# Kernel tuning notes

Hardware: AMD Instinct MI355X
Metric: run time of the kernel (lower is better)

## Reference

```python
import jax, jax.numpy as jnp
import numpy as np

N_HEAD = 16
N_EMBD = 2048
HEAD_DIM = N_EMBD // N_HEAD  # 128
ROPE_THETA = 10000.0


def _make_rope(T, hd, theta):
    inv = 1.0 / (theta ** (np.arange(0, hd, 2, dtype=np.float32) / hd))  # (hd/2,)
    t = np.arange(T, dtype=np.float32)
    freqs = np.outer(t, inv)  # (T, hd/2)
    return jnp.asarray(np.cos(freqs)), jnp.asarray(np.sin(freqs))


def setup_inputs() -> dict:
    key = jax.random.key(0)
    k1, k2, k3 = jax.random.split(key, 3)
    B, T, C = 2, 2048, N_EMBD
    x = jax.random.normal(k1, (B, T, C), dtype=jnp.float32)
    cos, sin = _make_rope(T, HEAD_DIM, ROPE_THETA)
    w_qkv = jax.random.normal(k2, (3 * C, C), dtype=jnp.float32) * (1.0 / np.sqrt(C))
    w_proj = jax.random.normal(k3, (C, C), dtype=jnp.float32) * (1.0 / np.sqrt(C))
    return {"x": x, "cos": cos, "sin": sin, "w_qkv": w_qkv, "w_proj": w_proj}


def _apply_rope(x, cos, sin):
    # x: (B, H, T, hd); cos/sin: (T, hd/2). Interleaved (even/odd) RoPE.
    B, H, T, hd = x.shape
    xp = x.reshape(B, H, T, hd // 2, 2)
    x1, x2 = xp[..., 0], xp[..., 1]
    c = cos[:T][None, None, :, :]
    s = sin[:T][None, None, :, :]
    even = x1 * c - x2 * s
    odd = x1 * s + x2 * c
    return jnp.stack([even, odd], axis=-1).reshape(B, H, T, hd)


def reference(x, cos, sin, w_qkv, w_proj):
    B, T, C = x.shape
    H, hd = N_HEAD, HEAD_DIM
    qkv = jnp.einsum('btc,dc->btd', x, w_qkv)  # (B,T,3C)
    q, k, v = jnp.split(qkv, 3, axis=-1)
    # (B,T,C) -> (B,H,T,hd)
    q = q.reshape(B, T, H, hd).transpose(0, 2, 1, 3)
    k = k.reshape(B, T, H, hd).transpose(0, 2, 1, 3)
    v = v.reshape(B, T, H, hd).transpose(0, 2, 1, 3)
    q = _apply_rope(q, cos, sin)
    k = _apply_rope(k, cos, sin)
    scale = 1.0 / jnp.sqrt(jnp.asarray(hd, dtype=x.dtype))
    scores = jnp.einsum('bhqd,bhkd->bhqk', q, k) * scale  # (B,H,T,T)
    causal = jnp.tril(jnp.ones((T, T), dtype=bool))
    scores = jnp.where(causal[None, None], scores, jnp.asarray(-jnp.inf, dtype=scores.dtype))
    attn = jax.nn.softmax(scores, axis=-1)
    out = jnp.einsum('bhqk,bhkd->bhqd', attn, v)  # (B,H,T,hd)
    out = out.transpose(0, 2, 1, 3).reshape(B, T, C)
    return jnp.einsum('btc,dc->btd', out, w_proj)
```

## Files before the change

### kernel.cpp

```cpp
#include <hip/hip_runtime.h>
#include <hip/hip_bf16.h>
#include <stdint.h>

typedef __attribute__((ext_vector_type(8))) short bf16x8;
typedef __attribute__((ext_vector_type(4))) float f32x4;

#define B_ 2
#define T_ 2048
#define C_ 2048
#define H_ 16
#define HD_ 128

__device__ inline ushort f2bf(float f) {
  union { float f; uint32_t u; } v; v.f = f;
  uint32_t u = v.u;
  uint32_t r = (u + 0x7fffu + ((u >> 16) & 1u)) >> 16;
  return (ushort)r;
}
__device__ inline float bf2f(ushort h) {
  union { uint32_t u; float f; } v; v.u = ((uint32_t)h) << 16;
  return v.f;
}

typedef const __attribute__((address_space(1))) void* gas1_t;
typedef __attribute__((address_space(3))) void* las3_t;
__device__ inline void gld_lds16(const void* g, void* l) {
  __builtin_amdgcn_global_load_lds((gas1_t)g, (las3_t)l, 16, 0, 0);
}

__global__ __launch_bounds__(256) void k_f2bf(const float* __restrict__ in,
                                              ushort* __restrict__ out, int n4) {
  int i = blockIdx.x * 256 + threadIdx.x;
  if (i < n4) {
    f32x4 v = *(const f32x4*)(in + (size_t)i * 4);
    ushort4 o;
    o.x = f2bf(v[0]); o.y = f2bf(v[1]); o.z = f2bf(v[2]); o.w = f2bf(v[3]);
    *(ushort4*)(out + (size_t)i * 4) = o;
  }
}

template <int OUT_BF16>
__global__ __launch_bounds__(256)
void gemm_bt(const ushort* __restrict__ A, const ushort* __restrict__ Bm,
             void* __restrict__ Cout, int M, int N, int K) {
  __shared__ ushort lA[2][128 * 32];
  __shared__ ushort lB[2][128 * 32];
  const int tid = threadIdx.x;
  const int wid = tid >> 6, lane = tid & 63;
  const int bx = blockIdx.x, by = blockIdx.y;
  const size_t rowA0 = (size_t)by * 128, colB0 = (size_t)bx * 128;
  const int sr = lane >> 2, sc = (lane & 3) * 8;

  const ushort* Abase = A + rowA0 * K + sc;
  const ushort* Bbase = Bm + colB0 * K + sc;

  auto stage = [&](int buf, int kt) {
    const ushort* Ak = Abase + (size_t)kt * 32;
    const ushort* Bk = Bbase + (size_t)kt * 32;
    for (int i = 0; i < 2; i++) {
      int chunk = wid * 2 + i;
      int row = chunk * 16 + sr;
      gld_lds16(Ak + (size_t)row * K, &lA[buf][chunk * 512]);
      gld_lds16(Bk + (size_t)row * K, &lB[buf][chunk * 512]);
    }
  };

  f32x4 acc[4][4];
  const f32x4 zf = {0.f, 0.f, 0.f, 0.f};
  for (int i = 0; i < 4; i++)
    for (int j = 0; j < 4; j++) acc[i][j] = zf;

  const int wr = (wid >> 1) * 64, wc = (wid & 1) * 64;
  const int lr = lane & 15, lk = (lane >> 4) * 8;

  stage(0, 0);
  __syncthreads();
  const int NT = K / 32;
  int buf = 0;
  for (int kt = 0; kt < NT; kt++) {
    if (kt + 1 < NT) stage(buf ^ 1, kt + 1);
    bf16x8 af[4], bfr[4];
    for (int i = 0; i < 4; i++)
      af[i] = *(const bf16x8*)&lA[buf][(wr + i * 16 + lr) * 32 + lk];
    for (int j = 0; j < 4; j++)
      bfr[j] = *(const bf16x8*)&lB[buf][(wc + j * 16 + lr) * 32 + lk];
    for (int i = 0; i < 4; i++)
      for (int j = 0; j < 4; j++)
        acc[i][j] = __builtin_amdgcn_mfma_f32_16x16x32_bf16(af[i], bfr[j],
                                                            acc[i][j], 0, 0, 0);
    __syncthreads();
    buf ^= 1;
  }
  const int lq = (lane >> 4) * 4;
  for (int i = 0; i < 4; i++)
    for (int j = 0; j < 4; j++)
      for (int r = 0; r < 4; r++) {
        size_t row = rowA0 + wr + i * 16 + lq + r;
        size_t col = colB0 + wc + j * 16 + lr;
        float v = acc[i][j][r];
        if (OUT_BF16)
          ((ushort*)Cout)[row * (size_t)N + col] = f2bf(v);
        else
          ((float*)Cout)[row * (size_t)N + col] = v;
      }
}

__global__ __launch_bounds__(256)
void rope_split(const ushort* __restrict__ qkv, const float* __restrict__ cosb,
                const float* __restrict__ sinb, ushort* __restrict__ Qr,
                ushort* __restrict__ Kr, ushort* __restrict__ Vr) {
  const int bt = blockIdx.x;
  const int b = bt >> 11, t = bt & 2047;
  const ushort* base = qkv + (size_t)bt * (3 * C_);
  const int tid = threadIdx.x;
  const float rs = 0.08838834764831845f;
  for (int i = 0; i < 4; i++) {
    int idx = tid + i * 256;
    int h = idx >> 6, p = idx & 63;
    float c = cosb[t * 64 + p], s = sinb[t * 64 + p];
    size_t src = (size_t)h * HD_ + 2 * p;
    size_t dst = (((size_t)(b * H_ + h)) * T_ + t) * HD_ + 2 * p;
    float x1 = bf2f(base[src]), x2 = bf2f(base[src + 1]);
    Qr[dst] = f2bf((x1 * c - x2 * s) * rs);
    Qr[dst + 1] = f2bf((x1 * s + x2 * c) * rs);
    x1 = bf2f(base[C_ + src]); x2 = bf2f(base[C_ + src + 1]);
    Kr[dst] = f2bf(x1 * c - x2 * s);
    Kr[dst + 1] = f2bf(x1 * s + x2 * c);
    Vr[dst] = base[2 * C_ + src];
    Vr[dst + 1] = base[2 * C_ + src + 1];
  }
}

__global__ __launch_bounds__(256)
void attn_fwd(const ushort* __restrict__ Qr, const ushort* __restrict__ Kr,
              const ushort* __restrict__ Vr, ushort* __restrict__ Out) {
  __shared__ ushort lK[32][136];
  __shared__ ushort lV[128][40];
  __shared__ ushort lP[4][16][40];
  const int tid = threadIdx.x, wid = tid >> 6, lane = tid & 63;
  const int bh = blockIdx.y;
  const int b = bh >> 4, h = bh & 15;
  const int qt = (blockIdx.x + blockIdx.y) & 31;
  const int qbase = qt * 64 + wid * 16;
  const int lr = lane & 15, lk8 = (lane >> 4) * 8;

  const ushort* Qp = Qr + ((size_t)bh * T_ + qbase) * HD_;
  const ushort* Kp = Kr + (size_t)bh * T_ * HD_;
  const ushort* Vp = Vr + (size_t)bh * T_ * HD_;

  bf16x8 qf[4];
  for (int dc = 0; dc < 4; dc++)
    qf[dc] = *(const bf16x8*)(Qp + (size_t)lr * HD_ + dc * 32 + lk8);

  f32x4 o[8];
  const f32x4 zf = {0.f, 0.f, 0.f, 0.f};
  for (int dt = 0; dt < 8; dt++) o[dt] = zf;
  float m[4], l[4];
  for (int r = 0; r < 4; r++) { m[r] = -1e30f; l[r] = 0.f; }

  int rK[2], cK[2], rV[2], cV[2];
  for (int i = 0; i < 2; i++) {
    int chunk = tid + i * 256;
    rK[i] = chunk >> 4; cK[i] = (chunk & 15) * 8;
    rV[i] = chunk & 31; cV[i] = (chunk >> 5) * 8;
  }

  bf16x8 kreg[2], vreg[2];
  auto load_tile = [&](int kt) {
    for (int i = 0; i < 2; i++) {
      kreg[i] = *(const bf16x8*)(Kp + ((size_t)(kt * 32 + rK[i])) * HD_ + cK[i]);
      vreg[i] = *(const bf16x8*)(Vp + ((size_t)(kt * 32 + rV[i])) * HD_ + cV[i]);
    }
  };

  const int nkt = 2 * qt + 2;
  load_tile(0);
  for (int kt = 0; kt < nkt; kt++) {
    __syncthreads();
    for (int i = 0; i < 2; i++) {
      *(bf16x8*)&lK[rK[i]][cK[i]] = kreg[i];
      for (int j = 0; j < 8; j++) lV[cV[i] + j][rV[i]] = (ushort)vreg[i][j];
    }
    if (kt + 1 < nkt) load_tile(kt + 1);
    __syncthreads();
    if (kt * 32 <= qbase + 15) {
      f32x4 s[2];
      for (int kn = 0; kn < 2; kn++) {
        f32x4 a = zf;
        for (int dc = 0; dc < 4; dc++) {
          bf16x8 kf = *(const bf16x8*)&lK[kn * 16 + lr][dc * 32 + lk8];
          a = __builtin_amdgcn_mfma_f32_16x16x32_bf16(qf[dc], kf, a, 0, 0, 0);
        }
        s[kn] = a;
      }
      const int qrow = qbase + (lane >> 4) * 4;
      for (int kn = 0; kn < 2; kn++) {
        int kg = kt * 32 + kn * 16 + lr;
        for (int r = 0; r < 4; r++)
          if (kg > qrow + r) s[kn][r] = -1e30f;
      }
      float al[4];
      for (int r = 0; r < 4; r++) {
        float pm = fmaxf(s[0][r], s[1][r]);
        for (int off = 1; off < 16; off <<= 1)
          pm = fmaxf(pm, __shfl_xor(pm, off, 64));
        float mn = fmaxf(m[r], pm);
        float a = __expf(m[r] - mn);
        float p0 = __expf(s[0][r] - mn);
        float p1 = __expf(s[1][r] - mn);
        s[0][r] = p0; s[1][r] = p1;
        float rsum = p0 + p1;
        for (int off = 1; off < 16; off <<= 1)
          rsum += __shfl_xor(rsum, off, 64);
        l[r] = l[r] * a + rsum;
        m[r] = mn;
        al[r] = a;
      }
      for (int dt = 0; dt < 8; dt++)
        for (int r = 0; r < 4; r++) o[dt][r] *= al[r];
      for (int kn = 0; kn < 2; kn++)
        for (int r = 0; r < 4; r++)
          lP[wid][(lane >> 4) * 4 + r][kn * 16 + lr] = f2bf(s[kn][r]);
      bf16x8 pf = *(const bf16x8*)&lP[wid][lr][lk8];
      for (int dt = 0; dt < 8; dt++) {
        bf16x8 vf = *(const bf16x8*)&lV[dt * 16 + lr][lk8];
        o[dt] = __builtin_amdgcn_mfma_f32_16x16x32_bf16(pf, vf, o[dt], 0, 0, 0);
      }
    }
  }
  for (int r = 0; r < 4; r++) {
    float inv = 1.0f / l[r];
    int qg = qbase + (lane >> 4) * 4 + r;
    size_t obase = ((size_t)b * T_ + qg) * C_ + (size_t)h * HD_;
    for (int dt = 0; dt < 8; dt++)
      Out[obase + dt * 16 + lr] = f2bf(o[dt][r] * inv);
  }
}

extern "C" void kernel_launch(void* const* d_in, const int* in_sizes, int n_in,
                              void* d_out, int out_size, void* d_ws,
                              size_t ws_size, hipStream_t stream) {
  (void)in_sizes; (void)n_in; (void)out_size; (void)ws_size;
  const float* x = (const float*)d_in[0];
  const float* cosb = (const float*)d_in[1];
  const float* sinb = (const float*)d_in[2];
  const float* w_qkv = (const float*)d_in[3];
  const float* w_proj = (const float*)d_in[4];

  char* ws = (char*)d_ws;
  ushort* wqkvb = (ushort*)(ws);
  ushort* wprojb = (ushort*)(ws + 25165824);
  ushort* xb = (ushort*)(ws + 25165824 + 8388608);
  ushort* qkv = (ushort*)(ws + 25165824 + 8388608 + 16777216);
  ushort* kr = (ushort*)(ws + 25165824 + 8388608 + 16777216 + 50331648);
  ushort* vr = (ushort*)(ws + 25165824 + 8388608 + 16777216 + 50331648 + 16777216);
  ushort* qr = xb;
  ushort* attn_out = qkv;

  k_f2bf<<<8192, 256, 0, stream>>>(x, xb, 2097152);
  k_f2bf<<<12288, 256, 0, stream>>>(w_qkv, wqkvb, 3145728);
  k_f2bf<<<4096, 256, 0, stream>>>(w_proj, wprojb, 1048576);

  gemm_bt<1><<<dim3(48, 32), 256, 0, stream>>>(xb, wqkvb, (void*)qkv,
                                               4096, 6144, 2048);
  rope_split<<<4096, 256, 0, stream>>>(qkv, cosb, sinb, qr, kr, vr);
  attn_fwd<<<dim3(32, 32), 256, 0, stream>>>(qr, kr, vr, attn_out);
  gemm_bt<0><<<dim3(16, 32), 256, 0, stream>>>(attn_out, wprojb, d_out,
                                               4096, 2048, 2048);
}
```

Before: 499.1 us.

## Pair causal q-tiles per block, transpose MFMA operands, add lazy softmax rescale

The attention kernel now runs 16 blocks per head, and each block handles q-tile pr and q-tile 31-pr in turn, so every block gets the same causal work. The QK and PV MFMAs swap operand order, which puts one query row in each lane. That turns the row max and sum reductions into two cross-group shuffles instead of four, and allows vectorized output and P stores. An online-softmax rescale is skipped when the new max exceeds the old one by no more than 5 in every lane, which avoids the per-tile accumulator scaling. The trade-offs are half as many blocks, which may lower occupancy and latency hiding, and some numerical risk from the deferred max.

```diff
diff --git a/kernel.cpp b/kernel.cpp
--- a/kernel.cpp
+++ b/kernel.cpp
@@ -140,23 +140,12 @@
   const int tid = threadIdx.x, wid = tid >> 6, lane = tid & 63;
   const int bh = blockIdx.y;
   const int b = bh >> 4, h = bh & 15;
-  const int qt = (blockIdx.x + blockIdx.y) & 31;
-  const int qbase = qt * 64 + wid * 16;
-  const int lr = lane & 15, lk8 = (lane >> 4) * 8;
-
-  const ushort* Qp = Qr + ((size_t)bh * T_ + qbase) * HD_;
+  const int pr = blockIdx.x;
+  const int lr = lane & 15, g = lane >> 4, lk8 = g * 8;
+  const f32x4 zf = {0.f, 0.f, 0.f, 0.f};
+
   const ushort* Kp = Kr + (size_t)bh * T_ * HD_;
   const ushort* Vp = Vr + (size_t)bh * T_ * HD_;
-
-  bf16x8 qf[4];
-  for (int dc = 0; dc < 4; dc++)
-    qf[dc] = *(const bf16x8*)(Qp + (size_t)lr * HD_ + dc * 32 + lk8);
-
-  f32x4 o[8];
-  const f32x4 zf = {0.f, 0.f, 0.f, 0.f};
-  for (int dt = 0; dt < 8; dt++) o[dt] = zf;
-  float m[4], l[4];
-  for (int r = 0; r < 4; r++) { m[r] = -1e30f; l[r] = 0.f; }
 
   int rK[2], cK[2], rV[2], cV[2];
   for (int i = 0; i < 2; i++) {
@@ -165,75 +154,103 @@
     rV[i] = chunk & 31; cV[i] = (chunk >> 5) * 8;
   }
 
-  bf16x8 kreg[2], vreg[2];
-  auto load_tile = [&](int kt) {
-    for (int i = 0; i < 2; i++) {
-      kreg[i] = *(const bf16x8*)(Kp + ((size_t)(kt * 32 + rK[i])) * HD_ + cK[i]);
-      vreg[i] = *(const bf16x8*)(Vp + ((size_t)(kt * 32 + rV[i])) * HD_ + cV[i]);
+  for (int seg = 0; seg < 2; ++seg) {
+    const int qt = seg ? (31 - pr) : pr;
+    const int qbase = qt * 64 + wid * 16;
+    const ushort* Qp = Qr + ((size_t)bh * T_ + qbase) * HD_;
+
+    bf16x8 qf[4];
+    for (int dc = 0; dc < 4; dc++)
+      qf[dc] = *(const bf16x8*)(Qp + (size_t)lr * HD_ + dc * 32 + lk8);
+
+    f32x4 o[8];
+    for (int dt = 0; dt < 8; dt++) o[dt] = zf;
+    float m = -1e30f, l = 0.f;
+
+    bf16x8 kreg[2], vreg[2];
+    auto load_tile = [&](int kt) {
+      for (int i = 0; i < 2; i++) {
+        kreg[i] = *(const bf16x8*)(Kp + ((size_t)(kt * 32 + rK[i])) * HD_ + cK[i]);
+        vreg[i] = *(const bf16x8*)(Vp + ((size_t)(kt * 32 + rV[i])) * HD_ + cV[i]);
+      }
+    };
+
+    const int nkt = 2 * qt + 2;
+    load_tile(0);
+    for (int kt = 0; kt < nkt; kt++) {
+      __syncthreads();
+      for (int i = 0; i < 2; i++) {
+        *(bf16x8*)&lK[rK[i]][cK[i]] = kreg[i];
+        for (int j = 0; j < 8; j++) lV[cV[i] + j][rV[i]] = (ushort)vreg[i][j];
+      }
+      if (kt + 1 < nkt) load_tile(kt + 1);
+      __syncthreads();
+      if (kt * 32 <= qbase + 15) {
+        f32x4 s[2];
+        for (int kn = 0; kn < 2; kn++) {
+          f32x4 a = zf;
+          for (int dc = 0; dc < 4; dc++) {
+            bf16x8 kf = *(const bf16x8*)&lK[kn * 16 + lr][dc * 32 + lk8];
+            a = __builtin_amdgcn_mfma_f32_16x16x32_bf16(kf, qf[dc], a, 0, 0, 0);
+          }
+          s[kn] = a;
+        }
+        const int qg = qbase + lr;
+        if (kt * 32 + 31 > qbase) {
+          for (int kn = 0; kn < 2; kn++) {
+            int k0 = kt * 32 + kn * 16 + g * 4;
+            for (int r = 0; r < 4; r++)
+              if (k0 + r > qg) s[kn][r] = -1e30f;
+          }
+        }
+        float pm = fmaxf(fmaxf(fmaxf(s[0][0], s[0][1]), fmaxf(s[0][2], s[0][3])),
+                         fmaxf(fmaxf(s[1][0], s[1][1]), fmaxf(s[1][2], s[1][3])));
+        pm = fmaxf(pm, __shfl_xor(pm, 16, 64));
+        pm = fmaxf(pm, __shfl_xor(pm, 32, 64));
+        if (!__all(pm - m <= 5.0f)) {
+          float mn = fmaxf(m, pm);
+          float a = __expf(m - mn);
+          for (int dt = 0; dt < 8; dt++)
+            for (int r = 0; r < 4; r++) o[dt][r] *= a;
+          l *= a;
+          m = mn;
+        }
+        float p[8];
+        float rsum = 0.f;
+        for (int kn = 0; kn < 2; kn++)
+          for (int r = 0; r < 4; r++) {
+            float pv = __expf(s[kn][r] - m);
+            p[kn * 4 + r] = pv;
+            rsum += pv;
+          }
+        rsum += __shfl_xor(rsum, 16, 64);
+        rsum += __shfl_xor(rsum, 32, 64);
+        l += rsum;
+        for (int kn = 0; kn < 2; kn++) {
+          ushort2 w0, w1;
+          w0.x = f2bf(p[kn * 4 + 0]); w0.y = f2bf(p[kn * 4 + 1]);
+          w1.x = f2bf(p[kn * 4 + 2]); w1.y = f2bf(p[kn * 4 + 3]);
+          *(ushort2*)&lP[wid][lr][kn * 16 + g * 4] = w0;
+          *(ushort2*)&lP[wid][lr][kn * 16 + g * 4 + 2] = w1;
+        }
+        bf16x8 pf = *(const bf16x8*)&lP[wid][lr][lk8];
+        for (int dt = 0; dt < 8; dt++) {
+          bf16x8 vf = *(const bf16x8*)&lV[dt * 16 + lr][lk8];
+          o[dt] = __builtin_amdgcn_mfma_f32_16x16x32_bf16(vf, pf, o[dt], 0, 0, 0);
+        }
+      }
     }
-  };
-
-  const int nkt = 2 * qt + 2;
-  load_tile(0);
-  for (int kt = 0; kt < nkt; kt++) {
-    __syncthreads();
-    for (int i = 0; i < 2; i++) {
-      *(bf16x8*)&lK[rK[i]][cK[i]] = kreg[i];
-      for (int j = 0; j < 8; j++) lV[cV[i] + j][rV[i]] = (ushort)vreg[i][j];
+    float inv = 1.0f / l;
+    int qg = qbase + lr;
+    size_t obase = ((size_t)b * T_ + qg) * C_ + (size_t)h * HD_;
+    for (int dt = 0; dt < 8; dt++) {
+      ushort4 w;
+      w.x = f2bf(o[dt][0] * inv);
+      w.y = f2bf(o[dt][1] * inv);
+      w.z = f2bf(o[dt][2] * inv);
+      w.w = f2bf(o[dt][3] * inv);
+      *(ushort4*)&Out[obase + dt * 16 + g * 4] = w;
     }
-    if (kt + 1 < nkt) load_tile(kt + 1);
-    __syncthreads();
-    if (kt * 32 <= qbase + 15) {
-      f32x4 s[2];
-      for (int kn = 0; kn < 2; kn++) {
-        f32x4 a = zf;
-        for (int dc = 0; dc < 4; dc++) {
-          bf16x8 kf = *(const bf16x8*)&lK[kn * 16 + lr][dc * 32 + lk8];
-          a = __builtin_amdgcn_mfma_f32_16x16x32_bf16(qf[dc], kf, a, 0, 0, 0);
-        }
-        s[kn] = a;
-      }
-      const int qrow = qbase + (lane >> 4) * 4;
-      for (int kn = 0; kn < 2; kn++) {
-        int kg = kt * 32 + kn * 16 + lr;
-        for (int r = 0; r < 4; r++)
-          if (kg > qrow + r) s[kn][r] = -1e30f;
-      }
-      float al[4];
-      for (int r = 0; r < 4; r++) {
-        float pm = fmaxf(s[0][r], s[1][r]);
-        for (int off = 1; off < 16; off <<= 1)
-          pm = fmaxf(pm, __shfl_xor(pm, off, 64));
-        float mn = fmaxf(m[r], pm);
-        float a = __expf(m[r] - mn);
-        float p0 = __expf(s[0][r] - mn);
-        float p1 = __expf(s[1][r] - mn);
-        s[0][r] = p0; s[1][r] = p1;
-        float rsum = p0 + p1;
-        for (int off = 1; off < 16; off <<= 1)
-          rsum += __shfl_xor(rsum, off, 64);
-        l[r] = l[r] * a + rsum;
-        m[r] = mn;
-        al[r] = a;
-      }
-      for (int dt = 0; dt < 8; dt++)
-        for (int r = 0; r < 4; r++) o[dt][r] *= al[r];
-      for (int kn = 0; kn < 2; kn++)
-        for (int r = 0; r < 4; r++)
-          lP[wid][(lane >> 4) * 4 + r][kn * 16 + lr] = f2bf(s[kn][r]);
-      bf16x8 pf = *(const bf16x8*)&lP[wid][lr][lk8];
-      for (int dt = 0; dt < 8; dt++) {
-        bf16x8 vf = *(const bf16x8*)&lV[dt * 16 + lr][lk8];
-        o[dt] = __builtin_amdgcn_mfma_f32_16x16x32_bf16(pf, vf, o[dt], 0, 0, 0);
-      }
-    }
-  }
-  for (int r = 0; r < 4; r++) {
-    float inv = 1.0f / l[r];
-    int qg = qbase + (lane >> 4) * 4 + r;
-    size_t obase = ((size_t)b * T_ + qg) * C_ + (size_t)h * HD_;
-    for (int dt = 0; dt < 8; dt++)
-      Out[obase + dt * 16 + lr] = f2bf(o[dt][r] * inv);
   }
 }
 
@@ -264,7 +281,7 @@
   gemm_bt<1><<<dim3(48, 32), 256, 0, stream>>>(xb, wqkvb, (void*)qkv,
                                                4096, 6144, 2048);
   rope_split<<<4096, 256, 0, stream>>>(qkv, cosb, sinb, qr, kr, vr);
-  attn_fwd<<<dim3(32, 32), 256, 0, stream>>>(qr, kr, vr, attn_out);
+  attn_fwd<<<dim3(16, 32), 256, 0, stream>>>(qr, kr, vr, attn_out);
   gemm_bt<0><<<dim3(16, 32), 256, 0, stream>>>(attn_out, wprojb, d_out,
                                                4096, 2048, 2048);
 }
```

New measurement: 410.8 us. 1.21x faster.
